# Optimization experiments

Hardware: AMD Instinct MI355X
Metric: run time of the kernel (lower is better)

## Reference

```python
import jax, jax.numpy as jnp
import numpy as np

N, C, T, H, W = 2, 512, 8, 28, 28
THW = T * H * W
BN_EPS = 1e-5


def conv1x1(x, Wt, b):
    # pointwise channel mixing, equivalent to 1x1 Conv2d/Conv3d on (N,C,T,H,W)
    return jnp.einsum('oc,ncthw->nothw', Wt, x) + b[None, :, None, None, None]


def setup_inputs() -> dict:
    key = jax.random.key(0)
    ks = jax.random.split(key, 8)
    s = 1.0 / np.sqrt(C)
    x = jax.random.normal(ks[0], (N, C, T, H, W), dtype=jnp.float32)
    mask = jax.random.uniform(ks[1], (N, C, T, H, W), dtype=jnp.float32)
    Wh = jax.random.normal(ks[2], (C, C), dtype=jnp.float32) * s
    Wg = jax.random.normal(ks[3], (C, C), dtype=jnp.float32) * s
    Wm = jax.random.normal(ks[4], (C, C), dtype=jnp.float32) * s
    Wz = jax.random.normal(ks[5], (C, C), dtype=jnp.float32) * s  # kaiming-like
    bh = jnp.zeros((C,), jnp.float32)
    bg = jnp.zeros((C,), jnp.float32)
    bm = jnp.zeros((C,), jnp.float32)
    bz = jnp.zeros((C,), jnp.float32)
    bn_w = jnp.ones((C,), jnp.float32)
    bn_b = jnp.zeros((C,), jnp.float32)
    gamma = jnp.float32(1.0)  # self.gamma (undefined in source __init__); learnable scalar
    return dict(x=x, mask=mask, Wh=Wh, bh=bh, Wg=Wg, bg=bg, Wm=Wm, bm=bm,
                Wz=Wz, bz=bz, bn_w=bn_w, bn_b=bn_b, gamma=gamma)


def reference(x, mask, Wh, bh, Wg, bg, Wm, bm, Wz, bz, bn_w, bn_b, gamma):
    n = x.shape[0]
    # proj_f = h(x) reshaped (N, THW, C); proj_g = g(x) (N, C, THW)
    ph_x = conv1x1(x, Wh, bh).reshape(n, C, THW)
    pg = conv1x1(x, Wg, bg).reshape(n, C, THW)
    # energy[n,t,s] = sum_c ph_x[n,c,t] * pg[n,c,s]  -> (N, THW, THW)
    energy = jnp.einsum('nct,ncs->nts', ph_x, pg)
    attention = jax.nn.softmax(energy, axis=-1)
    # proj_h uses self.h on mask (faithful to source)
    ph_m = conv1x1(mask, Wh, bh).reshape(n, C, THW)
    # bmm(proj_h, attention^T): [n,c,t] = sum_s ph_m[n,c,s] * attention[n,t,s]
    mask_energy = jnp.einsum('ncs,nts->nct', ph_m, attention)
    mask_atten = jax.nn.softmax(mask_energy, axis=-1)  # softmax over THW
    pm = conv1x1(x, Wm, bm)
    out = pm * mask_atten.reshape(n, C, T, H, W)
    # W_z: 1x1 Conv3d + BatchNorm3d (training-mode batch stats, weight=1, bias=0)
    wy = conv1x1(x, Wz, bz)
    mu = jnp.mean(wy, axis=(0, 2, 3, 4), keepdims=True)
    var = jnp.var(wy, axis=(0, 2, 3, 4), keepdims=True)
    wy = (wy - mu) * jax.lax.rsqrt(var + BN_EPS)
    wy = wy * bn_w[None, :, None, None, None] + bn_b[None, :, None, None, None]
    return gamma * out + wy
```

## Files before the change

### kernel.cpp

```cpp
#include <hip/hip_runtime.h>
#include <hip/hip_bf16.h>
#include <math.h>

#define NN 2
#define CC 512
#define PP 6272
#define TCHMAX 1664
#define NCHK 4
#define NJT 49
#define EM 64.0f
static const size_t PPC = (size_t)PP * CC;
static const size_t NCP = (size_t)NN * PPC;

typedef unsigned short ushortT;
typedef __attribute__((ext_vector_type(8))) short short8;
typedef __attribute__((ext_vector_type(4))) float f32x4;

#define WAITV(N) asm volatile("s_waitcnt vmcnt(" #N ")" ::: "memory")
#define BAR() __builtin_amdgcn_s_barrier()

__device__ __forceinline__ ushortT f2bf(float f) {
  __hip_bfloat16 h = __float2bfloat16(f);
  return *reinterpret_cast<ushortT*>(&h);
}
__device__ __forceinline__ float bf2f(ushortT u) {
  return __uint_as_float(((unsigned)u) << 16);
}

__device__ __forceinline__ void ld_g2l(const void* g, void* l) {
  __builtin_amdgcn_global_load_lds(
      (const __attribute__((address_space(1))) void*)g,
      (__attribute__((address_space(3))) void*)l, 16, 0, 0);
}

__device__ __forceinline__ int xcd_remap(int orig, int nwg) {
  const int q = nwg >> 3, r = nwg & 7;
  const int x = orig & 7, lo = orig >> 3;
  return (x < r) ? x * (q + 1) + lo : r * (q + 1) + (x - r) * q + lo;
}


__global__ __launch_bounds__(256) void k_prep(const float* __restrict__ x,
                                              const float* __restrict__ mask,
                                              const float* __restrict__ W0,
                                              const float* __restrict__ W1,
                                              const float* __restrict__ W2,
                                              const float* __restrict__ W3,
                                              ushortT* __restrict__ Wbf,
                                              ushortT* __restrict__ xT,
                                              ushortT* __restrict__ maskT) {
  __shared__ float T[32][33];
  const int tid = threadIdx.x;
  int b = blockIdx.x;
  if (b < 1024) {
    const int by = b >> 8, bx = b & 255;
    const float* src = (by == 0) ? W0 : (by == 1) ? W1 : (by == 2) ? W2 : W3;
    const int i = (bx * 256 + tid) * 4;
    float4 v = *(const float4*)&src[i];
    ushort4 o;
    o.x = f2bf(v.x); o.y = f2bf(v.y); o.z = f2bf(v.z); o.w = f2bf(v.w);
    *(ushort4*)&Wbf[(size_t)by * CC * CC + i] = o;
    return;
  }
  b -= 1024;
  const int bx = b % 196;
  const int by = (b / 196) & 15;
  const int zz = b / (196 * 16);
  const float* in = (zz < 2) ? x : mask;
  ushortT* out = (zz < 2) ? xT : maskT;
  const int p0 = bx * 32, c0 = by * 32;
  const int tx = tid & 31, ty = tid >> 5;
  const size_t nbi = (size_t)(zz & 1) * PPC;
#pragma unroll
  for (int i = 0; i < 4; ++i)
    T[ty + i * 8][tx] = in[nbi + (size_t)(c0 + ty + i * 8) * PP + p0 + tx];
  __syncthreads();
#pragma unroll
  for (int i = 0; i < 4; ++i) {
    int r = ty + i * 8;
    out[nbi + (size_t)(p0 + r) * CC + c0 + tx] = f2bf(T[tx][r]);
  }
}

__global__ __launch_bounds__(256, 2) void k_convs(
    const ushortT* __restrict__ xT, const ushortT* __restrict__ maskT,
    const ushortT* __restrict__ Whbf, const ushortT* __restrict__ Wgbf,
    const ushortT* __restrict__ Wmbf, const ushortT* __restrict__ Wzbf,
    const float* __restrict__ bh, const float* __restrict__ bg,
    const float* __restrict__ bm, const float* __restrict__ bz,
    ushortT* __restrict__ phxT, ushortT* __restrict__ pgT,
    ushortT* __restrict__ phmB, ushortT* __restrict__ pmB,
    ushortT* __restrict__ wzb) {
  __shared__ __align__(16) ushortT smem[36864];
  const int tid = threadIdx.x;
  const int l = tid & 63, w = tid >> 6;
  const int orig = blockIdx.x;
  const int wgid = (orig & 7) * 147 + (orig >> 3);
  const int zq = wgid / 196;
  const int within = wgid % 196;
  const int ctile = within & 3;
  const int ptile = within >> 2;
  const int wA = (w & 1) * 64, wB = (w >> 1) * 64;
  const int lr = l & 15, lk = l >> 4;
  const int r4 = (l >> 4) * 4;
  const int srow = l >> 2;
  const int sg8 = ((l & 3) ^ ((l >> 3) & 3)) * 8;
  const int rg16 = (lk ^ ((lr >> 1) & 3)) * 16;

  int offL[4], offR[4];
#pragma unroll
  for (int t = 0; t < 4; ++t) {
    offL[t] = (wA + t * 16 + lr) * 64 + rg16;
    offR[t] = (wB + t * 16 + lr) * 64 + rg16;
  }

  auto stage = [&](const ushortT* src, ushortT* dst) {
#pragma unroll
    for (int i = 0; i < 2; ++i)
      ld_g2l(src + (size_t)(w * 32 + i * 16 + srow) * CC + sg8,
             (char*)dst + (w * 2 + i) * 1024);
  };
  auto ldf = [&](const ushortT* base, const int* off, short8* f) {
#pragma unroll
    for (int t = 0; t < 4; ++t)
      f[t] = *(const short8*)((const char*)base + off[t]);
  };

  ushortT* Ca = smem;          ushortT* Na = smem + 4096;  ushortT* Za = smem + 8192;
  ushortT* Cb = smem + 12288;  ushortT* Nb = smem + 16384; ushortT* Zb = smem + 20480;
  ushortT* Cc = smem + 24576;  ushortT* Nc = smem + 28672; ushortT* Zc = smem + 32768;

  if (zq < 2) {
    const int zb = zq;
    const int p0 = ptile * 128, c0 = ctile * 128;
    const ushortT* Ax = xT + (size_t)zb * PPC + (size_t)p0 * CC;
    const ushortT* Bw1 = Whbf + (size_t)c0 * CC;
    const ushortT* Bw2 = Wgbf + (size_t)c0 * CC;
    ushortT* o1 = phxT + (size_t)zb * PPC;
    ushortT* o2 = pgT + (size_t)zb * PPC;
    f32x4 a1[4][4] = {}, a2[4][4] = {};
    stage(Ax, Ca); stage(Bw1, Cb); stage(Bw2, Cc);
    stage(Ax + 32, Na); stage(Bw1 + 32, Nb); stage(Bw2 + 32, Nc);
    WAITV(6); BAR();
    for (int t = 0; t < 16; ++t) {
      if (t < 14) {
        const int k = (t + 2) * 32;
        stage(Ax + k, Za); stage(Bw1 + k, Zb); stage(Bw2 + k, Zc);
      }
      short8 fp[4], fw[4];
      ldf(Ca, offL, fp);
      ldf(Cb, offR, fw);
      __builtin_amdgcn_s_setprio(1);
#pragma unroll
      for (int ss = 0; ss < 4; ++ss)
#pragma unroll
        for (int tt = 0; tt < 4; ++tt)
          a1[ss][tt] = __builtin_amdgcn_mfma_f32_16x16x32_bf16(fw[ss], fp[tt], a1[ss][tt], 0, 0, 0);
      __builtin_amdgcn_s_setprio(0);
      ldf(Cc, offR, fw);
      __builtin_amdgcn_s_setprio(1);
#pragma unroll
      for (int ss = 0; ss < 4; ++ss)
#pragma unroll
        for (int tt = 0; tt < 4; ++tt)
          a2[ss][tt] = __builtin_amdgcn_mfma_f32_16x16x32_bf16(fw[ss], fp[tt], a2[ss][tt], 0, 0, 0);
      __builtin_amdgcn_s_setprio(0);
      if (t < 14) { WAITV(6); } else { WAITV(0); }
      BAR();
      ushortT* tp;
      tp = Ca; Ca = Na; Na = Za; Za = tp;
      tp = Cb; Cb = Nb; Nb = Zb; Zb = tp;
      tp = Cc; Cc = Nc; Nc = Zc; Zc = tp;
    }
#pragma unroll
    for (int tt = 0; tt < 4; ++tt) {
      const size_t prow = (size_t)(p0 + wA + tt * 16 + lr) * CC;
#pragma unroll
      for (int ss = 0; ss < 4; ++ss) {
        const int co = c0 + wB + ss * 16 + r4;
        float4 b1v = *(const float4*)&bh[co];
        float4 b2v = *(const float4*)&bg[co];
        ushort4 v1, v2;
        v1.x = f2bf(a1[ss][tt][0] + b1v.x);
        v1.y = f2bf(a1[ss][tt][1] + b1v.y);
        v1.z = f2bf(a1[ss][tt][2] + b1v.z);
        v1.w = f2bf(a1[ss][tt][3] + b1v.w);
        v2.x = f2bf(a2[ss][tt][0] + b2v.x);
        v2.y = f2bf(a2[ss][tt][1] + b2v.y);
        v2.z = f2bf(a2[ss][tt][2] + b2v.z);
        v2.w = f2bf(a2[ss][tt][3] + b2v.w);
        *(ushort4*)&o1[prow + co] = v1;
        *(ushort4*)&o2[prow + co] = v2;
      }
    }
  } else if (zq < 4) {
    const int zb = zq - 2;
    const int s0 = ptile * 128, c0 = ctile * 128;
    const ushortT* Am = maskT + (size_t)zb * PPC + (size_t)s0 * CC;
    const ushortT* Bw = Whbf + (size_t)c0 * CC;
    ushortT* o = phmB + (size_t)zb * PPC;
    f32x4 a[4][4] = {};
    stage(Am, Ca); stage(Bw, Cb);
    stage(Am + 32, Na); stage(Bw + 32, Nb);
    WAITV(4); BAR();
    for (int t = 0; t < 16; ++t) {
      if (t < 14) {
        const int k = (t + 2) * 32;
        stage(Am + k, Za); stage(Bw + k, Zb);
      }
      short8 fs[4], fc[4];
      ldf(Ca, offL, fs);
      ldf(Cb, offR, fc);
      __builtin_amdgcn_s_setprio(1);
#pragma unroll
      for (int ss = 0; ss < 4; ++ss)
#pragma unroll
        for (int tt = 0; tt < 4; ++tt)
          a[ss][tt] = __builtin_amdgcn_mfma_f32_16x16x32_bf16(fs[ss], fc[tt], a[ss][tt], 0, 0, 0);
      __builtin_amdgcn_s_setprio(0);
      if (t < 14) { WAITV(4); } else { WAITV(0); }
      BAR();
      ushortT* tp;
      tp = Ca; Ca = Na; Na = Za; Za = tp;
      tp = Cb; Cb = Nb; Nb = Zb; Zb = tp;
    }
#pragma unroll
    for (int tt = 0; tt < 4; ++tt) {
      const int c = c0 + wB + tt * 16 + lr;
      const float bi = bh[c];
      const size_t crow = (size_t)c * PP;
#pragma unroll
      for (int ss = 0; ss < 4; ++ss) {
        ushort4 v;
        v.x = f2bf(a[ss][tt][0] + bi);
        v.y = f2bf(a[ss][tt][1] + bi);
        v.z = f2bf(a[ss][tt][2] + bi);
        v.w = f2bf(a[ss][tt][3] + bi);
        *(ushort4*)&o[crow + s0 + wA + ss * 16 + r4] = v;
      }
    }
  } else {
    const int zb = zq - 4;
    const int p0 = ptile * 128, c0 = ctile * 128;
    const ushortT* Ax = xT + (size_t)zb * PPC + (size_t)p0 * CC;
    const ushortT* Bw1 = Wmbf + (size_t)c0 * CC;
    const ushortT* Bw2 = Wzbf + (size_t)c0 * CC;
    ushortT* o1 = pmB + (size_t)zb * PPC;
    ushortT* o2 = wzb + (size_t)zb * PPC;
    f32x4 a1[4][4] = {}, a2[4][4] = {};
    stage(Ax, Ca); stage(Bw1, Cb); stage(Bw2, Cc);
    stage(Ax + 32, Na); stage(Bw1 + 32, Nb); stage(Bw2 + 32, Nc);
    WAITV(6); BAR();
    for (int t = 0; t < 16; ++t) {
      if (t < 14) {
        const int k = (t + 2) * 32;
        stage(Ax + k, Za); stage(Bw1 + k, Zb); stage(Bw2 + k, Zc);
      }
      short8 fx[4], fw[4];
      ldf(Ca, offL, fx);
      ldf(Cb, offR, fw);
      __builtin_amdgcn_s_setprio(1);
#pragma unroll
      for (int ss = 0; ss < 4; ++ss)
#pragma unroll
        for (int tt = 0; tt < 4; ++tt)
          a1[ss][tt] = __builtin_amdgcn_mfma_f32_16x16x32_bf16(fx[ss], fw[tt], a1[ss][tt], 0, 0, 0);
      __builtin_amdgcn_s_setprio(0);
      ldf(Cc, offR, fw);
      __builtin_amdgcn_s_setprio(1);
#pragma unroll
      for (int ss = 0; ss < 4; ++ss)
#pragma unroll
        for (int tt = 0; tt < 4; ++tt)
          a2[ss][tt] = __builtin_amdgcn_mfma_f32_16x16x32_bf16(fx[ss], fw[tt], a2[ss][tt], 0, 0, 0);
      __builtin_amdgcn_s_setprio(0);
      if (t < 14) { WAITV(6); } else { WAITV(0); }
      BAR();
      ushortT* tp;
      tp = Ca; Ca = Na; Na = Za; Za = tp;
      tp = Cb; Cb = Nb; Nb = Zb; Zb = tp;
      tp = Cc; Cc = Nc; Nc = Zc; Zc = tp;
    }
#pragma unroll
    for (int tt = 0; tt < 4; ++tt) {
      const int c = c0 + wB + tt * 16 + lr;
      const float b1v = bm[c], b2v = bz[c];
      const size_t crow = (size_t)c * PP;
#pragma unroll
      for (int ss = 0; ss < 4; ++ss) {
        const size_t off = crow + p0 + wA + ss * 16 + r4;
        ushort4 v1, v2;
        v1.x = f2bf(a1[ss][tt][0] + b1v);
        v1.y = f2bf(a1[ss][tt][1] + b1v);
        v1.z = f2bf(a1[ss][tt][2] + b1v);
        v1.w = f2bf(a1[ss][tt][3] + b1v);
        v2.x = f2bf(a2[ss][tt][0] + b2v);
        v2.y = f2bf(a2[ss][tt][1] + b2v);
        v2.z = f2bf(a2[ss][tt][2] + b2v);
        v2.w = f2bf(a2[ss][tt][3] + b2v);
        *(ushort4*)&o1[off] = v1;
        *(ushort4*)&o2[off] = v2;
      }
    }
  }
}

template <int KSPT>
__global__ __launch_bounds__(256, 3) void k_eadd(
    const ushortT* __restrict__ phxT, const ushortT* __restrict__ pgT,
    ushortT* __restrict__ Ech, float* __restrict__ Estat,
    int tbaseE, int tilesE, int nE,
    const ushortT* __restrict__ mePart, const float* __restrict__ rowZ,
    ushortT* __restrict__ meb, int tbaseM, int rowsM) {
  __shared__ __align__(16) ushortT smem[24576];
  __shared__ float Ss[128][2];
  const int tid = threadIdx.x;
  if ((int)blockIdx.x >= nE) {
    const int total4 = NN * CC * rowsM / 4;
    for (int e4 = ((int)blockIdx.x - nE) * 256 + tid; e4 < total4; e4 += 65536) {
      const int idx = e4 * 4;
      const int tl = idx % rowsM;
      const int c = (idx / rowsM) % CC;
      const int z = idx / (rowsM * CC);
      float s0 = 0.f, s1 = 0.f, s2 = 0.f, s3 = 0.f;
#pragma unroll
      for (int ks = 0; ks < KSPT; ++ks) {
        const size_t o = ((size_t)(ks * NN + z) * CC + c) * TCHMAX + tl;
        ushort4 a = *(const ushort4*)&mePart[o];
        s0 += bf2f(a.x); s1 += bf2f(a.y); s2 += bf2f(a.z); s3 += bf2f(a.w);
      }
      const float4 rz = *(const float4*)&rowZ[z * TCHMAX + tl];
      ushort4 v;
      v.x = f2bf(s0 * rz.x); v.y = f2bf(s1 * rz.y);
      v.z = f2bf(s2 * rz.z); v.w = f2bf(s3 * rz.w);
      *(ushort4*)&meb[((size_t)z * CC + c) * PP + tbaseM + tl] = v;
    }
    return;
  }
  const int l = tid & 63, w = tid >> 6;
  const int orig = blockIdx.x;
  const int wgid = xcd_remap(orig, NJT * tilesE * NN);
  const int it = wgid % tilesE;
  const int jt = (wgid / tilesE) % NJT;
  const int z = wgid / (tilesE * NJT);
  const int j0 = jt * 128;
  const int i0 = it * 128;
  const ushortT* Arow = phxT + (size_t)z * PPC + (size_t)(tbaseE + i0) * CC;
  const ushortT* Brow = pgT + (size_t)z * PPC + (size_t)j0 * CC;
  ushortT* out = Ech + (size_t)z * TCHMAX * PP;
  const int wi = (w & 1) * 64, wj = (w >> 1) * 64;
  const int lr = l & 15, lk = l >> 4;
  const int r4 = (l >> 4) * 4;
  const int srow = l >> 2;
  const int sg8 = ((l & 3) ^ ((l >> 3) & 3)) * 8;
  const int rg16 = (lk ^ ((lr >> 1) & 3)) * 16;

  int offA[4], offB[4];
#pragma unroll
  for (int t = 0; t < 4; ++t) {
    offA[t] = (wi + t * 16 + lr) * 64 + rg16;
    offB[t] = (wj + t * 16 + lr) * 64 + rg16;
  }
  auto stage = [&](const ushortT* src, ushortT* dst) {
#pragma unroll
    for (int i = 0; i < 2; ++i)
      ld_g2l(src + (size_t)(w * 32 + i * 16 + srow) * CC + sg8,
             (char*)dst + (w * 2 + i) * 1024);
  };

  ushortT* Ac = smem;          ushortT* An = smem + 4096;  ushortT* Az = smem + 8192;
  ushortT* Bc = smem + 12288;  ushortT* Bn = smem + 16384; ushortT* Bz = smem + 20480;

  f32x4 acc[4][4] = {};

  stage(Arow, Ac); stage(Brow, Bc);
  stage(Arow + 32, An); stage(Brow + 32, Bn);
  WAITV(4); BAR();
  for (int t = 0; t < 16; ++t) {
    if (t < 14) {
      const int k = (t + 2) * 32;
      stage(Arow + k, Az); stage(Brow + k, Bz);
    }
    short8 af[4], bfv[4];
#pragma unroll
    for (int tt = 0; tt < 4; ++tt)
      af[tt] = *(const short8*)((const char*)Ac + offA[tt]);
#pragma unroll
    for (int ss = 0; ss < 4; ++ss)
      bfv[ss] = *(const short8*)((const char*)Bc + offB[ss]);
    __builtin_amdgcn_s_setprio(1);
#pragma unroll
    for (int ss = 0; ss < 4; ++ss)
#pragma unroll
      for (int tt = 0; tt < 4; ++tt)
        acc[ss][tt] = __builtin_amdgcn_mfma_f32_16x16x32_bf16(bfv[ss], af[tt], acc[ss][tt], 0, 0, 0);
    __builtin_amdgcn_s_setprio(0);
    if (t < 14) { WAITV(4); } else { WAITV(0); }
    BAR();
    ushortT* tp;
    tp = Ac; Ac = An; An = Az; Az = tp;
    tp = Bc; Bc = Bn; Bn = Bz; Bz = tp;
  }
#pragma unroll
  for (int tt = 0; tt < 4; ++tt) {
    const int trow = i0 + wi + tt * 16 + lr;
    ushortT* orow = out + (size_t)trow * PP + j0;
    float sx = 0.f;
#pragma unroll
    for (int ss = 0; ss < 4; ++ss) {
      float u0 = __expf(acc[ss][tt][0] - EM);
      float u1 = __expf(acc[ss][tt][1] - EM);
      float u2 = __expf(acc[ss][tt][2] - EM);
      float u3 = __expf(acc[ss][tt][3] - EM);
      sx += (u0 + u1) + (u2 + u3);
      ushort4 v;
      v.x = f2bf(u0); v.y = f2bf(u1); v.z = f2bf(u2); v.w = f2bf(u3);
      *(ushort4*)&orow[wj + ss * 16 + r4] = v;
    }
    sx += __shfl_xor(sx, 16);
    sx += __shfl_xor(sx, 32);
    if (l < 16) Ss[wi + tt * 16 + l][w >> 1] = sx;
  }
  __syncthreads();
  if (tid < 128) {
    Estat[((size_t)z * TCHMAX + i0 + tid) * NJT + jt] = Ss[tid][0] + Ss[tid][1];
  }
}

template <int KSPT>
__global__ __launch_bounds__(256, 3) void k_mezc(
    const ushortT* __restrict__ phmB, const ushortT* __restrict__ Ech,
    ushortT* __restrict__ mePart, int gxM, int nM,
    const float* __restrict__ Estat, float* __restrict__ rowZ, int rows) {
  __shared__ __align__(16) ushortT smem[24576];
  const int tid = threadIdx.x;
  if ((int)blockIdx.x >= nM) {
    const int r = ((int)blockIdx.x - nM) * 256 + tid;
    if (r >= NN * rows) return;
    const int z = r / rows, tl = r % rows;
    const float* p = Estat + ((size_t)z * TCHMAX + tl) * NJT;
    float s = 0.f;
#pragma unroll
    for (int j = 0; j < NJT; ++j) s += p[j];
    rowZ[z * TCHMAX + tl] = 1.0f / s;
    return;
  }
  const int l = tid & 63, w = tid >> 6;
  const int orig = blockIdx.x;
  const int nwg = gxM * 4 * (NN * KSPT);
  const int wgid = (orig & 7) * (nwg >> 3) + (orig >> 3);
  const int cb = wgid & 3;
  const int tl = (wgid >> 2) % gxM;
  const int bz = (wgid >> 2) / gxM;
  const int tl0 = tl * 128;
  const int c0 = cb * 128;
  const int z = bz / KSPT, ks = bz % KSPT;
  const ushortT* Arow = phmB + (size_t)z * PPC + (size_t)c0 * PP;
  const ushortT* Brow = Ech + (size_t)z * TCHMAX * PP + (size_t)tl0 * PP;
  const int wc = (w & 1) * 64, wt = (w >> 1) * 64;
  const int lr = l & 15, lk = l >> 4;
  const int r4 = (l >> 4) * 4;
  const int srow = l >> 2;
  const int sg8 = ((l & 3) ^ ((l >> 3) & 3)) * 8;
  const int rg16 = (lk ^ ((lr >> 1) & 3)) * 16;

  int offA[4], offB[4];
#pragma unroll
  for (int t = 0; t < 4; ++t) {
    offA[t] = (wc + t * 16 + lr) * 64 + rg16;
    offB[t] = (wt + t * 16 + lr) * 64 + rg16;
  }

  auto st128 = [&](const ushortT* src, ushortT* dst) {
#pragma unroll
    for (int i = 0; i < 2; ++i)
      ld_g2l(src + (size_t)(w * 32 + i * 16 + srow) * PP + sg8,
             (char*)dst + (w * 2 + i) * 1024);
  };

  ushortT* Ac = smem;          ushortT* An = smem + 4096;  ushortT* Az = smem + 8192;
  ushortT* Bc = smem + 12288;  ushortT* Bn = smem + 16384; ushortT* Bz = smem + 20480;

  f32x4 acc[4][4] = {};

  const int sBeg = ((ks * 98) / KSPT) * 64;
  const int sEnd = (((ks + 1) * 98) / KSPT) * 64;
  const int NT = (sEnd - sBeg) >> 5;

  st128(Arow + sBeg, Ac); st128(Brow + sBeg, Bc);
  st128(Arow + sBeg + 32, An); st128(Brow + sBeg + 32, Bn);
  WAITV(4); BAR();
  for (int t = 0; t < NT; ++t) {
    if (t + 2 < NT) {
      const int k = sBeg + (t + 2) * 32;
      st128(Arow + k, Az); st128(Brow + k, Bz);
    }
    short8 af[4], bfv[4];
#pragma unroll
    for (int ct = 0; ct < 4; ++ct)
      af[ct] = *(const short8*)((const char*)Ac + offA[ct]);
#pragma unroll
    for (int tt = 0; tt < 4; ++tt)
      bfv[tt] = *(const short8*)((const char*)Bc + offB[tt]);
    __builtin_amdgcn_s_setprio(1);
#pragma unroll
    for (int tt = 0; tt < 4; ++tt)
#pragma unroll
      for (int ct = 0; ct < 4; ++ct)
        acc[tt][ct] = __builtin_amdgcn_mfma_f32_16x16x32_bf16(bfv[tt], af[ct], acc[tt][ct], 0, 0, 0);
    __builtin_amdgcn_s_setprio(0);
    if (t + 2 < NT) { WAITV(4); } else { WAITV(0); }
    BAR();
    ushortT* tp;
    tp = Ac; Ac = An; An = Az; Az = tp;
    tp = Bc; Bc = Bn; Bn = Bz; Bz = tp;
  }
  ushortT* out = mePart + ((size_t)(ks * NN + z) * CC) * TCHMAX;
#pragma unroll
  for (int ct = 0; ct < 4; ++ct) {
    const size_t crow = (size_t)(c0 + wc + ct * 16 + lr) * TCHMAX + tl0;
#pragma unroll
    for (int tt = 0; tt < 4; ++tt) {
      ushort4 v;
      v.x = f2bf(acc[tt][ct][0]);
      v.y = f2bf(acc[tt][ct][1]);
      v.z = f2bf(acc[tt][ct][2]);
      v.w = f2bf(acc[tt][ct][3]);
      *(ushort4*)&out[crow + wt + tt * 16 + r4] = v;
    }
  }
}

template <int KSPT>
__global__ __launch_bounds__(256) void k_meadd(const ushortT* __restrict__ mePart,
                                               const float* __restrict__ rowZ,
                                               ushortT* __restrict__ meb,
                                               int tbase, int rows) {
  const int idx = (blockIdx.x * 256 + threadIdx.x) * 4;
  const int tl = idx % rows;
  const int c = (idx / rows) % CC;
  const int z = idx / (rows * CC);
  float s0 = 0.f, s1 = 0.f, s2 = 0.f, s3 = 0.f;
#pragma unroll
  for (int ks = 0; ks < KSPT; ++ks) {
    const size_t o = ((size_t)(ks * NN + z) * CC + c) * TCHMAX + tl;
    ushort4 a = *(const ushort4*)&mePart[o];
    s0 += bf2f(a.x); s1 += bf2f(a.y); s2 += bf2f(a.z); s3 += bf2f(a.w);
  }
  const float4 rz = *(const float4*)&rowZ[z * TCHMAX + tl];
  ushort4 v;
  v.x = f2bf(s0 * rz.x); v.y = f2bf(s1 * rz.y);
  v.z = f2bf(s2 * rz.z); v.w = f2bf(s3 * rz.w);
  *(ushort4*)&meb[((size_t)z * CC + c) * PP + tbase + tl] = v;
}

__global__ __launch_bounds__(256) void k_stats(const ushortT* __restrict__ me,
                                               const ushortT* __restrict__ wz,
                                               float* __restrict__ m2,
                                               float* __restrict__ Z2,
                                               float* __restrict__ mu,
                                               float* __restrict__ rinv) {
  __shared__ float red[256];
  __shared__ float rq[256];
  const int tid = threadIdx.x;
  const int NCH = PP / 8;
  if ((int)blockIdx.x < NN * CC) {
    const ushortT* row = me + (size_t)blockIdx.x * PP;
    float m = -INFINITY;
    for (int i = tid; i < NCH; i += 256) {
      short8 v = *(const short8*)&row[i * 8];
#pragma unroll
      for (int j = 0; j < 8; ++j) m = fmaxf(m, bf2f((ushortT)v[j]));
    }
    red[tid] = m;
    __syncthreads();
    for (int s = 128; s > 0; s >>= 1) {
      if (tid < s) red[tid] = fmaxf(red[tid], red[tid + s]);
      __syncthreads();
    }
    m = red[0];
    __syncthreads();
    float zz = 0.f;
    for (int i = tid; i < NCH; i += 256) {
      short8 v = *(const short8*)&row[i * 8];
#pragma unroll
      for (int j = 0; j < 8; ++j) zz += __expf(bf2f((ushortT)v[j]) - m);
    }
    red[tid] = zz;
    __syncthreads();
    for (int s = 128; s > 0; s >>= 1) {
      if (tid < s) red[tid] += red[tid + s];
      __syncthreads();
    }
    if (tid == 0) { m2[blockIdx.x] = m; Z2[blockIdx.x] = red[0]; }
  } else {
    const int c = blockIdx.x - NN * CC;
    float s = 0.f, q = 0.f;
    for (int n = 0; n < NN; ++n) {
      const ushortT* rowp = wz + (size_t)n * CC * PP + (size_t)c * PP;
      for (int i = tid; i < NCH; i += 256) {
        short8 v = *(const short8*)&rowp[i * 8];
#pragma unroll
        for (int j = 0; j < 8; ++j) {
          float f = bf2f((ushortT)v[j]);
          s += f;
          q += f * f;
        }
      }
    }
    red[tid] = s; rq[tid] = q;
    __syncthreads();
    for (int st = 128; st > 0; st >>= 1) {
      if (tid < st) { red[tid] += red[tid + st]; rq[tid] += rq[tid + st]; }
      __syncthreads();
    }
    if (tid == 0) {
      const float inv_n = 1.0f / (float)(NN * PP);
      float mean = red[0] * inv_n;
      float var = rq[0] * inv_n - mean * mean;
      mu[c] = mean;
      rinv[c] = rsqrtf(var + 1e-5f);
    }
  }
}

__global__ __launch_bounds__(256) void k_final(const ushortT* __restrict__ pmB,
                                               const ushortT* __restrict__ me,
                                               const ushortT* __restrict__ wz,
                                               const float* __restrict__ m2,
                                               const float* __restrict__ Z2,
                                               const float* __restrict__ mu,
                                               const float* __restrict__ rinv,
                                               const float* __restrict__ bnw,
                                               const float* __restrict__ bnb,
                                               const float* __restrict__ gamma,
                                               float* __restrict__ out) {
  const int e4 = blockIdx.x * 256 + threadIdx.x;
  const size_t e = (size_t)e4 * 4;
  const int nc = (int)(e / PP);
  const int c = nc & (CC - 1);
  const float m = m2[nc];
  const float rz = 1.0f / Z2[nc];
  const float mub = mu[c];
  const float ri = rinv[c] * bnw[c];
  const float bb = bnb[c];
  const float g = gamma[0];
  ushort4 pv = *(const ushort4*)&pmB[e];
  ushort4 mev = *(const ushort4*)&me[e];
  ushort4 wzv = *(const ushort4*)&wz[e];
  float4 o;
  o.x = g * bf2f(pv.x) * (__expf(bf2f(mev.x) - m) * rz) + (bf2f(wzv.x) - mub) * ri + bb;
  o.y = g * bf2f(pv.y) * (__expf(bf2f(mev.y) - m) * rz) + (bf2f(wzv.y) - mub) * ri + bb;
  o.z = g * bf2f(pv.z) * (__expf(bf2f(mev.z) - m) * rz) + (bf2f(wzv.z) - mub) * ri + bb;
  o.w = g * bf2f(pv.w) * (__expf(bf2f(mev.w) - m) * rz) + (bf2f(wzv.w) - mub) * ri + bb;
  *(float4*)&out[e] = o;
}

extern "C" void kernel_launch(void* const* d_in, const int* in_sizes, int n_in,
                              void* d_out, int out_size, void* d_ws, size_t ws_size,
                              hipStream_t stream) {
  (void)in_sizes; (void)n_in; (void)out_size;
  const float* x    = (const float*)d_in[0];
  const float* mask = (const float*)d_in[1];
  const float* Wh   = (const float*)d_in[2];
  const float* bh   = (const float*)d_in[3];
  const float* Wg   = (const float*)d_in[4];
  const float* bg   = (const float*)d_in[5];
  const float* Wm   = (const float*)d_in[6];
  const float* bm   = (const float*)d_in[7];
  const float* Wz   = (const float*)d_in[8];
  const float* bz   = (const float*)d_in[9];
  const float* bnw  = (const float*)d_in[10];
  const float* bnb  = (const float*)d_in[11];
  const float* gam  = (const float*)d_in[12];

  ushortT* wzb  = (ushortT*)d_ws;
  ushortT* meb  = wzb + NCP;
  ushortT* pmB  = meb + NCP;
  ushortT* phxT = pmB + NCP;
  ushortT* pgT  = phxT + NCP;
  ushortT* phmB = pgT + NCP;
  ushortT* Wbf  = phmB + NCP;
  ushortT* Whbf = Wbf;
  ushortT* Wgbf = Wbf + 1 * CC * CC;
  ushortT* Wmbf = Wbf + 2 * CC * CC;
  ushortT* Wzbf = Wbf + 3 * CC * CC;
  float* m2    = (float*)(Wbf + 4 * CC * CC);
  float* Z2    = m2 + NN * CC;
  float* mu    = Z2 + NN * CC;
  float* rin   = mu + CC;
  float* Estat = rin + CC;
  float* rowZ  = Estat + (size_t)NN * TCHMAX * NJT;
  float* region = rowZ + (size_t)NN * TCHMAX + 16;
  ushortT* xT    = (ushortT*)region;
  ushortT* maskT = xT + NCP;
  ushortT* Ech    = (ushortT*)region;
  ushortT* mePart = Ech + (size_t)NN * TCHMAX * PP;

  const size_t regionOffB = (size_t)((char*)region - (char*)d_ws);
  const size_t need8 = regionOffB +
      ((size_t)NN * TCHMAX * PP + 8ull * NN * CC * TCHMAX) * 2;
  const bool k8 = ws_size >= need8;

  k_prep<<<1024 + 196 * 16 * 4, 256, 0, stream>>>(x, mask, Wh, Wg, Wm, Wz,
                                                  Wbf, xT, maskT);

  k_convs<<<1176, 256, 0, stream>>>(xT, maskT, Whbf, Wgbf, Wmbf, Wzbf,
                                    bh, bg, bm, bz, phxT, pgT, phmB, pmB, wzb);

  static const int chunkTiles[NCHK] = {13, 12, 12, 12};
  int tb[NCHK];
  {
    int acc = 0;
    for (int ch = 0; ch < NCHK; ++ch) { tb[ch] = acc; acc += chunkTiles[ch] * 128; }
  }
  const int KSPv = k8 ? 8 : 4;
  {
    const int nE = NJT * chunkTiles[0] * NN;
    if (k8)
      k_eadd<8><<<nE, 256, 0, stream>>>(phxT, pgT, Ech, Estat, tb[0],
                                        chunkTiles[0], nE, mePart, rowZ, meb, 0, 0);
    else
      k_eadd<4><<<nE, 256, 0, stream>>>(phxT, pgT, Ech, Estat, tb[0],
                                        chunkTiles[0], nE, mePart, rowZ, meb, 0, 0);
  }
  for (int ch = 0; ch < NCHK; ++ch) {
    const int rows = chunkTiles[ch] * 128;
    const int gxM = rows / 128;
    const int nM = gxM * 4 * NN * KSPv;
    const int zcB = (NN * rows + 255) / 256;
    if (k8)
      k_mezc<8><<<nM + zcB, 256, 0, stream>>>(phmB, Ech, mePart, gxM, nM,
                                              Estat, rowZ, rows);
    else
      k_mezc<4><<<nM + zcB, 256, 0, stream>>>(phmB, Ech, mePart, gxM, nM,
                                              Estat, rowZ, rows);
    if (ch < NCHK - 1) {
      const int tilesN = chunkTiles[ch + 1];
      const int nE = NJT * tilesN * NN;
      if (k8)
        k_eadd<8><<<nE + 256, 256, 0, stream>>>(phxT, pgT, Ech, Estat, tb[ch + 1],
                                                tilesN, nE, mePart, rowZ, meb,
                                                tb[ch], rows);
      else
        k_eadd<4><<<nE + 256, 256, 0, stream>>>(phxT, pgT, Ech, Estat, tb[ch + 1],
                                                tilesN, nE, mePart, rowZ, meb,
                                                tb[ch], rows);
    } else {
      if (k8)
        k_meadd<8><<<NN * CC * rows / 1024, 256, 0, stream>>>(mePart, rowZ, meb,
                                                              tb[ch], rows);
      else
        k_meadd<4><<<NN * CC * rows / 1024, 256, 0, stream>>>(mePart, rowZ, meb,
                                                              tb[ch], rows);
    }
  }

  k_stats<<<NN * CC + CC, 256, 0, stream>>>(meb, wzb, m2, Z2, mu, rin);
  const int total4 = (int)(NCP / 4);
  k_final<<<total4 / 256, 256, 0, stream>>>(pmB, meb, wzb, m2, Z2, mu, rin,
                                            bnw, bnb, gam, (float*)d_out);
}
```

Measured before the change: 485.0 us.

## Fuse attention stages into one mega-kernel with double-buffered chunk pipeline

```diff
diff --git a/kernel.cpp b/kernel.cpp
--- a/kernel.cpp
+++ b/kernel.cpp
@@ -5,9 +5,15 @@
 #define NN 2
 #define CC 512
 #define PP 6272
-#define TCHMAX 1664
-#define NCHK 4
+#define TCH 896
+#define NCHK 7
+#define TILES 7
 #define NJT 49
+#define KSP 4
+#define NE 686
+#define NM 224
+#define ZCB 7
+#define MAB 256
 #define EM 64.0f
 static const size_t PPC = (size_t)PP * CC;
 static const size_t NCP = (size_t)NN * PPC;
@@ -305,253 +311,222 @@
   }
 }
 
-template <int KSPT>
-__global__ __launch_bounds__(256, 3) void k_eadd(
+__global__ __launch_bounds__(256, 3) void k_mega(
     const ushortT* __restrict__ phxT, const ushortT* __restrict__ pgT,
-    ushortT* __restrict__ Ech, float* __restrict__ Estat,
-    int tbaseE, int tilesE, int nE,
-    const ushortT* __restrict__ mePart, const float* __restrict__ rowZ,
-    ushortT* __restrict__ meb, int tbaseM, int rowsM) {
+    ushortT* __restrict__ EchW, float* __restrict__ EstatW, int tbaseE, int nE,
+    const ushortT* __restrict__ phmB, const ushortT* __restrict__ EchR,
+    ushortT* __restrict__ mePartW, int nM,
+    const float* __restrict__ EstatR, float* __restrict__ rowZW, int zcB,
+    const ushortT* __restrict__ mePartR, const float* __restrict__ rowZR,
+    ushortT* __restrict__ meb, int tbaseA, int maB) {
   __shared__ __align__(16) ushortT smem[24576];
   __shared__ float Ss[128][2];
   const int tid = threadIdx.x;
-  if ((int)blockIdx.x >= nE) {
-    const int total4 = NN * CC * rowsM / 4;
-    for (int e4 = ((int)blockIdx.x - nE) * 256 + tid; e4 < total4; e4 += 65536) {
-      const int idx = e4 * 4;
-      const int tl = idx % rowsM;
-      const int c = (idx / rowsM) % CC;
-      const int z = idx / (rowsM * CC);
-      float s0 = 0.f, s1 = 0.f, s2 = 0.f, s3 = 0.f;
-#pragma unroll
-      for (int ks = 0; ks < KSPT; ++ks) {
-        const size_t o = ((size_t)(ks * NN + z) * CC + c) * TCHMAX + tl;
-        ushort4 a = *(const ushort4*)&mePart[o];
-        s0 += bf2f(a.x); s1 += bf2f(a.y); s2 += bf2f(a.z); s3 += bf2f(a.w);
-      }
-      const float4 rz = *(const float4*)&rowZ[z * TCHMAX + tl];
-      ushort4 v;
-      v.x = f2bf(s0 * rz.x); v.y = f2bf(s1 * rz.y);
-      v.z = f2bf(s2 * rz.z); v.w = f2bf(s3 * rz.w);
-      *(ushort4*)&meb[((size_t)z * CC + c) * PP + tbaseM + tl] = v;
-    }
-    return;
-  }
+  int bid = blockIdx.x;
   const int l = tid & 63, w = tid >> 6;
-  const int orig = blockIdx.x;
-  const int wgid = xcd_remap(orig, NJT * tilesE * NN);
-  const int it = wgid % tilesE;
-  const int jt = (wgid / tilesE) % NJT;
-  const int z = wgid / (tilesE * NJT);
-  const int j0 = jt * 128;
-  const int i0 = it * 128;
-  const ushortT* Arow = phxT + (size_t)z * PPC + (size_t)(tbaseE + i0) * CC;
-  const ushortT* Brow = pgT + (size_t)z * PPC + (size_t)j0 * CC;
-  ushortT* out = Ech + (size_t)z * TCHMAX * PP;
-  const int wi = (w & 1) * 64, wj = (w >> 1) * 64;
   const int lr = l & 15, lk = l >> 4;
   const int r4 = (l >> 4) * 4;
   const int srow = l >> 2;
   const int sg8 = ((l & 3) ^ ((l >> 3) & 3)) * 8;
   const int rg16 = (lk ^ ((lr >> 1) & 3)) * 16;
 
-  int offA[4], offB[4];
-#pragma unroll
-  for (int t = 0; t < 4; ++t) {
-    offA[t] = (wi + t * 16 + lr) * 64 + rg16;
-    offB[t] = (wj + t * 16 + lr) * 64 + rg16;
-  }
-  auto stage = [&](const ushortT* src, ushortT* dst) {
-#pragma unroll
-    for (int i = 0; i < 2; ++i)
-      ld_g2l(src + (size_t)(w * 32 + i * 16 + srow) * CC + sg8,
-             (char*)dst + (w * 2 + i) * 1024);
-  };
-
-  ushortT* Ac = smem;          ushortT* An = smem + 4096;  ushortT* Az = smem + 8192;
-  ushortT* Bc = smem + 12288;  ushortT* Bn = smem + 16384; ushortT* Bz = smem + 20480;
-
-  f32x4 acc[4][4] = {};
-
-  stage(Arow, Ac); stage(Brow, Bc);
-  stage(Arow + 32, An); stage(Brow + 32, Bn);
-  WAITV(4); BAR();
-  for (int t = 0; t < 16; ++t) {
-    if (t < 14) {
-      const int k = (t + 2) * 32;
-      stage(Arow + k, Az); stage(Brow + k, Bz);
-    }
-    short8 af[4], bfv[4];
-#pragma unroll
-    for (int tt = 0; tt < 4; ++tt)
-      af[tt] = *(const short8*)((const char*)Ac + offA[tt]);
-#pragma unroll
-    for (int ss = 0; ss < 4; ++ss)
-      bfv[ss] = *(const short8*)((const char*)Bc + offB[ss]);
-    __builtin_amdgcn_s_setprio(1);
-#pragma unroll
-    for (int ss = 0; ss < 4; ++ss)
+  if (bid < nE) {
+    const int orig = bid;
+    const int wgid = xcd_remap(orig, NE);
+    const int it = wgid % TILES;
+    const int jt = (wgid / TILES) % NJT;
+    const int z = wgid / (TILES * NJT);
+    const int j0 = jt * 128;
+    const int i0 = it * 128;
+    const ushortT* Arow = phxT + (size_t)z * PPC + (size_t)(tbaseE + i0) * CC;
+    const ushortT* Brow = pgT + (size_t)z * PPC + (size_t)j0 * CC;
+    ushortT* out = EchW + (size_t)z * TCH * PP;
+    const int wi = (w & 1) * 64, wj = (w >> 1) * 64;
+
+    int offA[4], offB[4];
+#pragma unroll
+    for (int t = 0; t < 4; ++t) {
+      offA[t] = (wi + t * 16 + lr) * 64 + rg16;
+      offB[t] = (wj + t * 16 + lr) * 64 + rg16;
+    }
+    auto stage = [&](const ushortT* src, ushortT* dst) {
+#pragma unroll
+      for (int i = 0; i < 2; ++i)
+        ld_g2l(src + (size_t)(w * 32 + i * 16 + srow) * CC + sg8,
+               (char*)dst + (w * 2 + i) * 1024);
+    };
+    ushortT* Ac = smem;          ushortT* An = smem + 4096;  ushortT* Az = smem + 8192;
+    ushortT* Bc = smem + 12288;  ushortT* Bn = smem + 16384; ushortT* Bz = smem + 20480;
+
+    f32x4 acc[4][4] = {};
+
+    stage(Arow, Ac); stage(Brow, Bc);
+    stage(Arow + 32, An); stage(Brow + 32, Bn);
+    WAITV(4); BAR();
+    for (int t = 0; t < 16; ++t) {
+      if (t < 14) {
+        const int k = (t + 2) * 32;
+        stage(Arow + k, Az); stage(Brow + k, Bz);
+      }
+      short8 af[4], bfv[4];
 #pragma unroll
       for (int tt = 0; tt < 4; ++tt)
-        acc[ss][tt] = __builtin_amdgcn_mfma_f32_16x16x32_bf16(bfv[ss], af[tt], acc[ss][tt], 0, 0, 0);
-    __builtin_amdgcn_s_setprio(0);
-    if (t < 14) { WAITV(4); } else { WAITV(0); }
-    BAR();
-    ushortT* tp;
-    tp = Ac; Ac = An; An = Az; Az = tp;
-    tp = Bc; Bc = Bn; Bn = Bz; Bz = tp;
-  }
-#pragma unroll
-  for (int tt = 0; tt < 4; ++tt) {
-    const int trow = i0 + wi + tt * 16 + lr;
-    ushortT* orow = out + (size_t)trow * PP + j0;
-    float sx = 0.f;
-#pragma unroll
-    for (int ss = 0; ss < 4; ++ss) {
-      float u0 = __expf(acc[ss][tt][0] - EM);
-      float u1 = __expf(acc[ss][tt][1] - EM);
-      float u2 = __expf(acc[ss][tt][2] - EM);
-      float u3 = __expf(acc[ss][tt][3] - EM);
-      sx += (u0 + u1) + (u2 + u3);
+        af[tt] = *(const short8*)((const char*)Ac + offA[tt]);
+#pragma unroll
+      for (int ss = 0; ss < 4; ++ss)
+        bfv[ss] = *(const short8*)((const char*)Bc + offB[ss]);
+      __builtin_amdgcn_s_setprio(1);
+#pragma unroll
+      for (int ss = 0; ss < 4; ++ss)
+#pragma unroll
+        for (int tt = 0; tt < 4; ++tt)
+          acc[ss][tt] = __builtin_amdgcn_mfma_f32_16x16x32_bf16(bfv[ss], af[tt], acc[ss][tt], 0, 0, 0);
+      __builtin_amdgcn_s_setprio(0);
+      if (t < 14) { WAITV(4); } else { WAITV(0); }
+      BAR();
+      ushortT* tp;
+      tp = Ac; Ac = An; An = Az; Az = tp;
+      tp = Bc; Bc = Bn; Bn = Bz; Bz = tp;
+    }
+#pragma unroll
+    for (int tt = 0; tt < 4; ++tt) {
+      const int trow = i0 + wi + tt * 16 + lr;
+      ushortT* orow = out + (size_t)trow * PP + j0;
+      float sx = 0.f;
+#pragma unroll
+      for (int ss = 0; ss < 4; ++ss) {
+        float u0 = __expf(acc[ss][tt][0] - EM);
+        float u1 = __expf(acc[ss][tt][1] - EM);
+        float u2 = __expf(acc[ss][tt][2] - EM);
+        float u3 = __expf(acc[ss][tt][3] - EM);
+        sx += (u0 + u1) + (u2 + u3);
+        ushort4 v;
+        v.x = f2bf(u0); v.y = f2bf(u1); v.z = f2bf(u2); v.w = f2bf(u3);
+        *(ushort4*)&orow[wj + ss * 16 + r4] = v;
+      }
+      sx += __shfl_xor(sx, 16);
+      sx += __shfl_xor(sx, 32);
+      if (l < 16) Ss[wi + tt * 16 + l][w >> 1] = sx;
+    }
+    __syncthreads();
+    if (tid < 128) {
+      EstatW[((size_t)z * TCH + i0 + tid) * NJT + jt] = Ss[tid][0] + Ss[tid][1];
+    }
+    return;
+  }
+  bid -= nE;
+  if (bid < nM) {
+    const int orig = bid;
+    const int wgid = (orig & 7) * (NM >> 3) + (orig >> 3);
+    const int cb = wgid & 3;
+    const int tl = (wgid >> 2) % TILES;
+    const int bz = (wgid >> 2) / TILES;
+    const int tl0 = tl * 128;
+    const int c0 = cb * 128;
+    const int z = bz / KSP, ks = bz % KSP;
+    const ushortT* Arow = phmB + (size_t)z * PPC + (size_t)c0 * PP;
+    const ushortT* Brow = EchR + (size_t)z * TCH * PP + (size_t)tl0 * PP;
+    const int wc = (w & 1) * 64, wt = (w >> 1) * 64;
+
+    int offA[4], offB[4];
+#pragma unroll
+    for (int t = 0; t < 4; ++t) {
+      offA[t] = (wc + t * 16 + lr) * 64 + rg16;
+      offB[t] = (wt + t * 16 + lr) * 64 + rg16;
+    }
+    auto st128 = [&](const ushortT* src, ushortT* dst) {
+#pragma unroll
+      for (int i = 0; i < 2; ++i)
+        ld_g2l(src + (size_t)(w * 32 + i * 16 + srow) * PP + sg8,
+               (char*)dst + (w * 2 + i) * 1024);
+    };
+    ushortT* Ac = smem;          ushortT* An = smem + 4096;  ushortT* Az = smem + 8192;
+    ushortT* Bc = smem + 12288;  ushortT* Bn = smem + 16384; ushortT* Bz = smem + 20480;
+
+    f32x4 acc[4][4] = {};
+
+    const int sBeg = ((ks * 98) / KSP) * 64;
+    const int sEnd = (((ks + 1) * 98) / KSP) * 64;
+    const int NT = (sEnd - sBeg) >> 5;
+
+    st128(Arow + sBeg, Ac); st128(Brow + sBeg, Bc);
+    st128(Arow + sBeg + 32, An); st128(Brow + sBeg + 32, Bn);
+    WAITV(4); BAR();
+    for (int t = 0; t < NT; ++t) {
+      if (t + 2 < NT) {
+        const int k = sBeg + (t + 2) * 32;
+        st128(Arow + k, Az); st128(Brow + k, Bz);
+      }
+      short8 af[4], bfv[4];
+#pragma unroll
+      for (int ct = 0; ct < 4; ++ct)
+        af[ct] = *(const short8*)((const char*)Ac + offA[ct]);
+#pragma unroll
+      for (int tt = 0; tt < 4; ++tt)
+        bfv[tt] = *(const short8*)((const char*)Bc + offB[tt]);
+      __builtin_amdgcn_s_setprio(1);
+#pragma unroll
+      for (int tt = 0; tt < 4; ++tt)
+#pragma unroll
+        for (int ct = 0; ct < 4; ++ct)
+          acc[tt][ct] = __builtin_amdgcn_mfma_f32_16x16x32_bf16(bfv[tt], af[ct], acc[tt][ct], 0, 0, 0);
+      __builtin_amdgcn_s_setprio(0);
+      if (t + 2 < NT) { WAITV(4); } else { WAITV(0); }
+      BAR();
+      ushortT* tp;
+      tp = Ac; Ac = An; An = Az; Az = tp;
+      tp = Bc; Bc = Bn; Bn = Bz; Bz = tp;
+    }
+    ushortT* out = mePartW + ((size_t)(ks * NN + z) * CC) * TCH;
+#pragma unroll
+    for (int ct = 0; ct < 4; ++ct) {
+      const size_t crow = (size_t)(c0 + wc + ct * 16 + lr) * TCH + tl0;
+#pragma unroll
+      for (int tt = 0; tt < 4; ++tt) {
+        ushort4 v;
+        v.x = f2bf(acc[tt][ct][0]);
+        v.y = f2bf(acc[tt][ct][1]);
+        v.z = f2bf(acc[tt][ct][2]);
+        v.w = f2bf(acc[tt][ct][3]);
+        *(ushort4*)&out[crow + wt + tt * 16 + r4] = v;
+      }
+    }
+    return;
+  }
+  bid -= nM;
+  if (bid < zcB) {
+    const int r = bid * 256 + tid;
+    if (r >= NN * TCH) return;
+    const int z = r / TCH, tl = r % TCH;
+    const float* p = EstatR + ((size_t)z * TCH + tl) * NJT;
+    float s = 0.f;
+#pragma unroll
+    for (int j = 0; j < NJT; ++j) s += p[j];
+    rowZW[z * TCH + tl] = 1.0f / s;
+    return;
+  }
+  bid -= zcB;
+  {
+    const int total4 = NN * CC * TCH / 4;
+    for (int e4 = bid * 256 + tid; e4 < total4; e4 += maB * 256) {
+      const int idx = e4 * 4;
+      const int tl = idx % TCH;
+      const int c = (idx / TCH) % CC;
+      const int z = idx / (TCH * CC);
+      float s0 = 0.f, s1 = 0.f, s2 = 0.f, s3 = 0.f;
+#pragma unroll
+      for (int ks = 0; ks < KSP; ++ks) {
+        const size_t o = ((size_t)(ks * NN + z) * CC + c) * TCH + tl;
+        ushort4 a = *(const ushort4*)&mePartR[o];
+        s0 += bf2f(a.x); s1 += bf2f(a.y); s2 += bf2f(a.z); s3 += bf2f(a.w);
+      }
+      const float4 rz = *(const float4*)&rowZR[z * TCH + tl];
       ushort4 v;
-      v.x = f2bf(u0); v.y = f2bf(u1); v.z = f2bf(u2); v.w = f2bf(u3);
-      *(ushort4*)&orow[wj + ss * 16 + r4] = v;
-    }
-    sx += __shfl_xor(sx, 16);
-    sx += __shfl_xor(sx, 32);
-    if (l < 16) Ss[wi + tt * 16 + l][w >> 1] = sx;
-  }
-  __syncthreads();
-  if (tid < 128) {
-    Estat[((size_t)z * TCHMAX + i0 + tid) * NJT + jt] = Ss[tid][0] + Ss[tid][1];
-  }
-}
-
-template <int KSPT>
-__global__ __launch_bounds__(256, 3) void k_mezc(
-    const ushortT* __restrict__ phmB, const ushortT* __restrict__ Ech,
-    ushortT* __restrict__ mePart, int gxM, int nM,
-    const float* __restrict__ Estat, float* __restrict__ rowZ, int rows) {
-  __shared__ __align__(16) ushortT smem[24576];
-  const int tid = threadIdx.x;
-  if ((int)blockIdx.x >= nM) {
-    const int r = ((int)blockIdx.x - nM) * 256 + tid;
-    if (r >= NN * rows) return;
-    const int z = r / rows, tl = r % rows;
-    const float* p = Estat + ((size_t)z * TCHMAX + tl) * NJT;
-    float s = 0.f;
-#pragma unroll
-    for (int j = 0; j < NJT; ++j) s += p[j];
-    rowZ[z * TCHMAX + tl] = 1.0f / s;
-    return;
-  }
-  const int l = tid & 63, w = tid >> 6;
-  const int orig = blockIdx.x;
-  const int nwg = gxM * 4 * (NN * KSPT);
-  const int wgid = (orig & 7) * (nwg >> 3) + (orig >> 3);
-  const int cb = wgid & 3;
-  const int tl = (wgid >> 2) % gxM;
-  const int bz = (wgid >> 2) / gxM;
-  const int tl0 = tl * 128;
-  const int c0 = cb * 128;
-  const int z = bz / KSPT, ks = bz % KSPT;
-  const ushortT* Arow = phmB + (size_t)z * PPC + (size_t)c0 * PP;
-  const ushortT* Brow = Ech + (size_t)z * TCHMAX * PP + (size_t)tl0 * PP;
-  const int wc = (w & 1) * 64, wt = (w >> 1) * 64;
-  const int lr = l & 15, lk = l >> 4;
-  const int r4 = (l >> 4) * 4;
-  const int srow = l >> 2;
-  const int sg8 = ((l & 3) ^ ((l >> 3) & 3)) * 8;
-  const int rg16 = (lk ^ ((lr >> 1) & 3)) * 16;
-
-  int offA[4], offB[4];
-#pragma unroll
-  for (int t = 0; t < 4; ++t) {
-    offA[t] = (wc + t * 16 + lr) * 64 + rg16;
-    offB[t] = (wt + t * 16 + lr) * 64 + rg16;
-  }
-
-  auto st128 = [&](const ushortT* src, ushortT* dst) {
-#pragma unroll
-    for (int i = 0; i < 2; ++i)
-      ld_g2l(src + (size_t)(w * 32 + i * 16 + srow) * PP + sg8,
-             (char*)dst + (w * 2 + i) * 1024);
-  };
-
-  ushortT* Ac = smem;          ushortT* An = smem + 4096;  ushortT* Az = smem + 8192;
-  ushortT* Bc = smem + 12288;  ushortT* Bn = smem + 16384; ushortT* Bz = smem + 20480;
-
-  f32x4 acc[4][4] = {};
-
-  const int sBeg = ((ks * 98) / KSPT) * 64;
-  const int sEnd = (((ks + 1) * 98) / KSPT) * 64;
-  const int NT = (sEnd - sBeg) >> 5;
-
-  st128(Arow + sBeg, Ac); st128(Brow + sBeg, Bc);
-  st128(Arow + sBeg + 32, An); st128(Brow + sBeg + 32, Bn);
-  WAITV(4); BAR();
-  for (int t = 0; t < NT; ++t) {
-    if (t + 2 < NT) {
-      const int k = sBeg + (t + 2) * 32;
-      st128(Arow + k, Az); st128(Brow + k, Bz);
-    }
-    short8 af[4], bfv[4];
-#pragma unroll
-    for (int ct = 0; ct < 4; ++ct)
-      af[ct] = *(const short8*)((const char*)Ac + offA[ct]);
-#pragma unroll
-    for (int tt = 0; tt < 4; ++tt)
-      bfv[tt] = *(const short8*)((const char*)Bc + offB[tt]);
-    __builtin_amdgcn_s_setprio(1);
-#pragma unroll
-    for (int tt = 0; tt < 4; ++tt)
-#pragma unroll
-      for (int ct = 0; ct < 4; ++ct)
-        acc[tt][ct] = __builtin_amdgcn_mfma_f32_16x16x32_bf16(bfv[tt], af[ct], acc[tt][ct], 0, 0, 0);
-    __builtin_amdgcn_s_setprio(0);
-    if (t + 2 < NT) { WAITV(4); } else { WAITV(0); }
-    BAR();
-    ushortT* tp;
-    tp = Ac; Ac = An; An = Az; Az = tp;
-    tp = Bc; Bc = Bn; Bn = Bz; Bz = tp;
-  }
-  ushortT* out = mePart + ((size_t)(ks * NN + z) * CC) * TCHMAX;
-#pragma unroll
-  for (int ct = 0; ct < 4; ++ct) {
-    const size_t crow = (size_t)(c0 + wc + ct * 16 + lr) * TCHMAX + tl0;
-#pragma unroll
-    for (int tt = 0; tt < 4; ++tt) {
-      ushort4 v;
-      v.x = f2bf(acc[tt][ct][0]);
-      v.y = f2bf(acc[tt][ct][1]);
-      v.z = f2bf(acc[tt][ct][2]);
-      v.w = f2bf(acc[tt][ct][3]);
-      *(ushort4*)&out[crow + wt + tt * 16 + r4] = v;
-    }
-  }
-}
-
-template <int KSPT>
-__global__ __launch_bounds__(256) void k_meadd(const ushortT* __restrict__ mePart,
-                                               const float* __restrict__ rowZ,
-                                               ushortT* __restrict__ meb,
-                                               int tbase, int rows) {
-  const int idx = (blockIdx.x * 256 + threadIdx.x) * 4;
-  const int tl = idx % rows;
-  const int c = (idx / rows) % CC;
-  const int z = idx / (rows * CC);
-  float s0 = 0.f, s1 = 0.f, s2 = 0.f, s3 = 0.f;
-#pragma unroll
-  for (int ks = 0; ks < KSPT; ++ks) {
-    const size_t o = ((size_t)(ks * NN + z) * CC + c) * TCHMAX + tl;
-    ushort4 a = *(const ushort4*)&mePart[o];
-    s0 += bf2f(a.x); s1 += bf2f(a.y); s2 += bf2f(a.z); s3 += bf2f(a.w);
-  }
-  const float4 rz = *(const float4*)&rowZ[z * TCHMAX + tl];
-  ushort4 v;
-  v.x = f2bf(s0 * rz.x); v.y = f2bf(s1 * rz.y);
-  v.z = f2bf(s2 * rz.z); v.w = f2bf(s3 * rz.w);
-  *(ushort4*)&meb[((size_t)z * CC + c) * PP + tbase + tl] = v;
+      v.x = f2bf(s0 * rz.x); v.y = f2bf(s1 * rz.y);
+      v.z = f2bf(s2 * rz.z); v.w = f2bf(s3 * rz.w);
+      *(ushort4*)&meb[((size_t)z * CC + c) * PP + tbaseA + tl] = v;
+    }
+  }
 }
 
 __global__ __launch_bounds__(256) void k_stats(const ushortT* __restrict__ me,
@@ -689,18 +664,19 @@
   float* Z2    = m2 + NN * CC;
   float* mu    = Z2 + NN * CC;
   float* rin   = mu + CC;
-  float* Estat = rin + CC;
-  float* rowZ  = Estat + (size_t)NN * TCHMAX * NJT;
-  float* region = rowZ + (size_t)NN * TCHMAX + 16;
+  const size_t ESTN = (size_t)NN * TCH * NJT;
+  float* Estat = rin + CC + 16;
+  float* rowZ  = Estat + 2 * ESTN;
+  float* region = rowZ + 2 * (size_t)NN * TCH + 16;
   ushortT* xT    = (ushortT*)region;
   ushortT* maskT = xT + NCP;
+  const size_t ECHN = (size_t)NN * TCH * PP;
+  const size_t MEPN = (size_t)KSP * NN * CC * TCH;
   ushortT* Ech    = (ushortT*)region;
-  ushortT* mePart = Ech + (size_t)NN * TCHMAX * PP;
-
-  const size_t regionOffB = (size_t)((char*)region - (char*)d_ws);
-  const size_t need8 = regionOffB +
-      ((size_t)NN * TCHMAX * PP + 8ull * NN * CC * TCHMAX) * 2;
-  const bool k8 = ws_size >= need8;
+  ushortT* mePart = Ech + 2 * ECHN;
+
+  const size_t needB = (size_t)((char*)(mePart + 2 * MEPN) - (char*)d_ws);
+  const bool dbuf = ws_size >= needB;
 
   k_prep<<<1024 + 196 * 16 * 4, 256, 0, stream>>>(x, mask, Wh, Wg, Wm, Wz,
                                                   Wbf, xT, maskT);
@@ -708,51 +684,50 @@
   k_convs<<<1176, 256, 0, stream>>>(xT, maskT, Whbf, Wgbf, Wmbf, Wzbf,
                                     bh, bg, bm, bz, phxT, pgT, phmB, pmB, wzb);
 
-  static const int chunkTiles[NCHK] = {13, 12, 12, 12};
-  int tb[NCHK];
-  {
-    int acc = 0;
-    for (int ch = 0; ch < NCHK; ++ch) { tb[ch] = acc; acc += chunkTiles[ch] * 128; }
-  }
-  const int KSPv = k8 ? 8 : 4;
-  {
-    const int nE = NJT * chunkTiles[0] * NN;
-    if (k8)
-      k_eadd<8><<<nE, 256, 0, stream>>>(phxT, pgT, Ech, Estat, tb[0],
-                                        chunkTiles[0], nE, mePart, rowZ, meb, 0, 0);
-    else
-      k_eadd<4><<<nE, 256, 0, stream>>>(phxT, pgT, Ech, Estat, tb[0],
-                                        chunkTiles[0], nE, mePart, rowZ, meb, 0, 0);
-  }
-  for (int ch = 0; ch < NCHK; ++ch) {
-    const int rows = chunkTiles[ch] * 128;
-    const int gxM = rows / 128;
-    const int nM = gxM * 4 * NN * KSPv;
-    const int zcB = (NN * rows + 255) / 256;
-    if (k8)
-      k_mezc<8><<<nM + zcB, 256, 0, stream>>>(phmB, Ech, mePart, gxM, nM,
-                                              Estat, rowZ, rows);
-    else
-      k_mezc<4><<<nM + zcB, 256, 0, stream>>>(phmB, Ech, mePart, gxM, nM,
-                                              Estat, rowZ, rows);
-    if (ch < NCHK - 1) {
-      const int tilesN = chunkTiles[ch + 1];
-      const int nE = NJT * tilesN * NN;
-      if (k8)
-        k_eadd<8><<<nE + 256, 256, 0, stream>>>(phxT, pgT, Ech, Estat, tb[ch + 1],
-                                                tilesN, nE, mePart, rowZ, meb,
-                                                tb[ch], rows);
-      else
-        k_eadd<4><<<nE + 256, 256, 0, stream>>>(phxT, pgT, Ech, Estat, tb[ch + 1],
-                                                tilesN, nE, mePart, rowZ, meb,
-                                                tb[ch], rows);
-    } else {
-      if (k8)
-        k_meadd<8><<<NN * CC * rows / 1024, 256, 0, stream>>>(mePart, rowZ, meb,
-                                                              tb[ch], rows);
-      else
-        k_meadd<4><<<NN * CC * rows / 1024, 256, 0, stream>>>(mePart, rowZ, meb,
-                                                              tb[ch], rows);
+  auto EchP = [&](int ch) { return Ech + (dbuf ? (size_t)(ch & 1) * ECHN : 0); };
+  auto EstP = [&](int ch) { return Estat + (dbuf ? (size_t)(ch & 1) * ESTN : 0); };
+  auto rzP  = [&](int ch) { return rowZ + (dbuf ? (size_t)(ch & 1) * NN * TCH : 0); };
+  auto mpP  = [&](int ch) { return mePart + (dbuf ? (size_t)(ch & 1) * MEPN : 0); };
+
+  if (dbuf) {
+    k_mega<<<NE, 256, 0, stream>>>(phxT, pgT, EchP(0), EstP(0), 0, NE,
+                                   phmB, nullptr, nullptr, 0,
+                                   nullptr, nullptr, 0,
+                                   nullptr, nullptr, meb, 0, 0);
+    for (int ch = 0; ch < NCHK; ++ch) {
+      const int hasE = (ch + 1 < NCHK);
+      const int hasA = (ch >= 1);
+      const int nE = hasE ? NE : 0;
+      const int maB = hasA ? MAB : 0;
+      k_mega<<<nE + NM + ZCB + maB, 256, 0, stream>>>(
+          phxT, pgT, EchP(ch + 1), EstP(ch + 1), (ch + 1) * TCH, nE,
+          phmB, EchP(ch), mpP(ch), NM,
+          EstP(ch), rzP(ch), ZCB,
+          mpP(ch - 1), rzP(ch - 1), meb, (ch - 1) * TCH, maB);
+    }
+    k_mega<<<MAB, 256, 0, stream>>>(phxT, pgT, nullptr, nullptr, 0, 0,
+                                    phmB, nullptr, nullptr, 0,
+                                    nullptr, nullptr, 0,
+                                    mpP(NCHK - 1), rzP(NCHK - 1), meb,
+                                    (NCHK - 1) * TCH, MAB);
+  } else {
+    k_mega<<<NE, 256, 0, stream>>>(phxT, pgT, EchP(0), EstP(0), 0, NE,
+                                   phmB, nullptr, nullptr, 0,
+                                   nullptr, nullptr, 0,
+                                   nullptr, nullptr, meb, 0, 0);
+    for (int ch = 0; ch < NCHK; ++ch) {
+      k_mega<<<NM + ZCB, 256, 0, stream>>>(
+          phxT, pgT, nullptr, nullptr, 0, 0,
+          phmB, EchP(ch), mpP(ch), NM,
+          EstP(ch), rzP(ch), ZCB,
+          nullptr, nullptr, meb, 0, 0);
+      const int hasE = (ch + 1 < NCHK);
+      const int nE = hasE ? NE : 0;
+      k_mega<<<nE + MAB, 256, 0, stream>>>(
+          phxT, pgT, EchP(ch + 1), EstP(ch + 1), (ch + 1) * TCH, nE,
+          phmB, nullptr, nullptr, 0,
+          nullptr, nullptr, 0,
+          mpP(ch), rzP(ch), meb, ch * TCH, MAB);
     }
   }
 
```

After: 574.2 us. +18.4%, slower.
